# Performance work log

Hardware: AMD Instinct MI355X
Metric: run time of the kernel (lower is better)

The kernel has to match this reference:

```python
import jax, jax.numpy as jnp
from jax import lax
import numpy as np

BATCH, SEQ_LEN, ENC_IN, C_OUT = 16, 512, 32, 32
N_ORDER = 256           # window_size
MULTISCALE = (1, 2, 4)
MODES = min(32, SEQ_LEN // 2)  # = 32


def make_hippo(N, dt):
    """HiPPO-LegT transition, bilinear (Tustin) discretization, Legendre eval matrix."""
    Q = np.arange(N, dtype=np.float64)
    R = (2 * Q + 1)[:, None]
    j, i = np.meshgrid(Q, Q)
    A = np.where(i < j, -1.0, (-1.0) ** (i - j + 1)) * R
    B = (-1.0) ** Q[:, None] * R                      # [N,1]
    I = np.eye(N)
    M = I - (dt / 2.0) * A
    Ad = np.linalg.solve(M, I + (dt / 2.0) * A)
    Bd = np.linalg.solve(M, dt * B).squeeze(-1)       # [N]
    vals = np.arange(0.0, 1.0, dt)
    x = 1.0 - 2.0 * vals
    P = np.zeros((N, len(vals)))
    P[0] = 1.0
    if N > 1:
        P[1] = x
    for n in range(1, N - 1):
        P[n + 1] = ((2 * n + 1) * x * P[n] - n * P[n - 1]) / (n + 1)
    E = P.T                                           # [len(vals), N]
    return Ad.astype(np.float32), Bd.astype(np.float32), E.astype(np.float32)


def setup_inputs():
    key = jax.random.key(0)
    ks = jax.random.split(key, 12)
    inp = {}
    inp['x_enc'] = jax.random.normal(ks[0], (BATCH, SEQ_LEN, ENC_IN), jnp.float32)
    inp['x_mark_enc'] = jax.random.normal(ks[1], (BATCH, SEQ_LEN, 4), jnp.float32)
    inp['x_dec'] = jax.random.normal(ks[2], (BATCH, SEQ_LEN, ENC_IN), jnp.float32)
    inp['x_mark_dec'] = jax.random.normal(ks[3], (BATCH, SEQ_LEN, 4), jnp.float32)
    inp['affine_weight'] = jnp.ones((1, 1, ENC_IN), jnp.float32)
    inp['affine_bias'] = jnp.zeros((1, 1, ENC_IN), jnp.float32)
    scale = 1.0 / (N_ORDER * N_ORDER)
    for s in range(3):
        inp[f'wr{s}'] = scale * jax.random.uniform(ks[4 + 2 * s], (N_ORDER, N_ORDER, MODES), jnp.float32)
        inp[f'wi{s}'] = scale * jax.random.uniform(ks[5 + 2 * s], (N_ORDER, N_ORDER, MODES), jnp.float32)
    inp['mlp_w'] = 0.1 * jax.random.normal(ks[10], (1, 3), jnp.float32)
    inp['mlp_b'] = jnp.zeros((1,), jnp.float32)
    inp['proj_w'] = 0.02 * jax.random.normal(ks[11], (ENC_IN, C_OUT), jnp.float32)
    inp['proj_b'] = jnp.zeros((C_OUT,), jnp.float32)
    for s, m in enumerate(MULTISCALE):
        A, Bv, E = make_hippo(N_ORDER, 1.0 / SEQ_LEN / m)
        inp[f'A{s}'] = jnp.asarray(A)
        inp[f'Bv{s}'] = jnp.asarray(Bv)
        inp[f'E{s}'] = jnp.asarray(E)
    return inp


def _hippo_scan(x, A, Bv):
    # x: [B, L, C] -> cs: [L, B, C, N]; c_t = A c_{t-1} + B f_t (applied on last dim)
    B_, L, C = x.shape
    c0 = jnp.zeros((B_, C, A.shape[0]), x.dtype)
    At = A.T
    def step(c, f):                      # f: [B, C]
        c = c @ At + f[..., None] * Bv
        return c, c
    _, cs = lax.scan(step, c0, jnp.transpose(x, (1, 0, 2)))
    return cs


def _spectral_conv(xc, wr, wi):
    # xc: [B, C, N, L]; keep first MODES rfft bins, complex channel mix over N, irfft
    L = xc.shape[-1]
    xf = jnp.fft.rfft(xc)                                # [B,C,N,L//2+1] complex64
    W = (wr + 1j * wi).astype(jnp.complex64)             # [N,N,MODES]
    out = jnp.einsum('bjix,iox->bjox', xf[..., :MODES], W)
    out_ft = jnp.pad(out, ((0, 0), (0, 0), (0, 0), (0, L // 2 + 1 - MODES)))
    return jnp.fft.irfft(out_ft, n=L)                    # [B,C,N,L]


def _forward(x_enc, affine_weight, affine_bias, specs, mlp_w, mlp_b, proj_w, proj_b, hippos):
    means = lax.stop_gradient(jnp.mean(x_enc, axis=1, keepdims=True))
    xc = x_enc - means
    stdev = lax.stop_gradient(jnp.sqrt(jnp.var(xc, axis=1, keepdims=True) + 1e-5))
    x = xc / stdev
    x = x * affine_weight + affine_bias                  # [B, L, C]
    pred_len = SEQ_LEN
    decs = []
    for (wr, wi), (A, Bv, E) in zip(specs, hippos):
        # multiscale slice x[:, -m*pred_len:] clips to full seq_len since pred_len==seq_len
        cs = _hippo_scan(x, A, Bv)                       # [L,B,C,N]
        x_in_c = jnp.transpose(cs, (1, 2, 3, 0))         # [B,C,N,L]
        out1 = _spectral_conv(x_in_c, wr, wi)            # [B,C,N,L]
        x_dec_c = out1[..., pred_len - 1]                # [B,C,N]
        dec = x_dec_c @ E[-pred_len:, :].T               # [B,C,pred_len]
        decs.append(dec)
    stacked = jnp.stack(decs, axis=-1)                   # [B,C,P,3]
    y = stacked @ mlp_w[0] + mlp_b[0]                    # Linear(3,1) + squeeze -> [B,C,P]
    y = jnp.transpose(y, (0, 2, 1))                      # [B,P,C]
    y = (y - affine_bias) / (affine_weight + 1e-10)
    y = y * stdev + means
    return y @ proj_w + proj_b                           # OutputBlock: per-step channel projection


def reference(x_enc, x_mark_enc, x_dec, x_mark_dec, affine_weight, affine_bias,
              wr0, wi0, wr1, wi1, wr2, wi2, mlp_w, mlp_b, proj_w, proj_b,
              A0, Bv0, E0, A1, Bv1, E1, A2, Bv2, E2):
    specs = [(wr0, wi0), (wr1, wi1), (wr2, wi2)]
    hippos = [(A0, Bv0, E0), (A1, Bv1, E1), (A2, Bv2, E2)]
    return _forward(x_enc, affine_weight, affine_bias, specs, mlp_w, mlp_b, proj_w, proj_b, hippos)
```

## Files before the change

### kernel.cpp

```cpp
#include <hip/hip_runtime.h>
#include <math.h>

#define SEQ 512
#define NORD 256
#define MODES 32
#define KBIG (NORD*MODES*2)
#define PI_F 3.14159265358979323846f

typedef _Float16 half8 __attribute__((ext_vector_type(8)));
typedef float floatx4 __attribute__((ext_vector_type(4)));
typedef unsigned int uint;



struct GJob {
  const float* A; const float* B; float* C; const float* scale_ptr;
  int M, N, lda, k0, k1, atomic;
};
struct GJobs {
  GJob j[6];
  const float* wwr[3]; const float* wwi[3];
  _Float16* Wt; int nGemm; int wb_i0; int wb_slab0;
};

__global__ __launch_bounds__(256) void gemm32_k(GJobs P) {
  int z = blockIdx.z;
  if (z >= P.nGemm) {
    if (blockIdx.y != 0) return;
    int ig = P.wb_i0 + (z - P.nGemm);
    int s = ig >> 8, i = ig & 255;
    const float* wr = P.wwr[s];
    const float* wi = P.wwi[s];
    uint* Wd = (uint*)(P.Wt + (size_t)(s - P.wb_slab0) * 4194304);
    int j = blockIdx.x * 256 + threadIdx.x;
    int ot = j >> 7, loc = j & 127;
    int ks = loc >> 6, kg8 = (loc >> 4) & 3, on = loc & 15;
    int o = ot * 16 + on, k0 = ks * 16 + kg8 * 4;
    float4 wr4 = *(const float4*)&wr[(size_t)i * 8192 + o * 32 + k0];
    float4 wi4 = *(const float4*)&wi[(size_t)i * 8192 + o * 32 + k0];
    float wa[4] = {wr4.x, wr4.y, wr4.z, wr4.w};
    float wb[4] = {wi4.x, wi4.y, wi4.z, wi4.w};
    uint out[4];
    #pragma unroll
    for (int q = 0; q < 4; q++) {
      int k = k0 + q;
      float sn, cn; __sincosf((2.f * PI_F / 512.f) * (float)k, &sn, &cn);
      float g = ((k == 0) ? (1.f / 512.f) : (2.f / 512.f)) * 4096.f;
      float v0 = g * (cn * wa[q] + sn * wb[q]);
      float v1 = g * (sn * wa[q] - cn * wb[q]);
      _Float16 h0 = (_Float16)v0, h1 = (_Float16)v1;
      unsigned short u0, u1;
      __builtin_memcpy(&u0, &h0, 2); __builtin_memcpy(&u1, &h1, 2);
      out[q] = (uint)u0 | ((uint)u1 << 16);
    }
    *(uint4*)&Wd[((size_t)(i * 16 + ot)) * 512 + loc * 4] = *(uint4*)out;
    return;
  }
  GJob jb = P.j[z];
  int col0 = blockIdx.x * 32;
  int row0 = blockIdx.y * 32;
  if (row0 >= jb.M || col0 >= jb.N) return;
  __shared__ float As[64][34];
  __shared__ float Bs[64][36];
  int tid = threadIdx.x;
  int tx = tid & 15, ty = tid >> 4;
  const float* A = jb.A; const float* B = jb.B;
  int M = jb.M, N = jb.N, lda = jb.lda;
  int kcA = (tid & 15) * 4, rA = tid >> 4;
  int ccB = (tid & 7) * 4, kkB = tid >> 3;
  int gr0 = row0 + rA, gr1 = row0 + rA + 16;
  const float4 z4 = make_float4(0.f, 0.f, 0.f, 0.f);
  float4 a0, a1, b0, b1;
  {
    int kb = jb.k0;
    a0 = (gr0 < M) ? *(const float4*)&A[(size_t)gr0 * lda + kb + kcA] : z4;
    a1 = (gr1 < M) ? *(const float4*)&A[(size_t)gr1 * lda + kb + kcA] : z4;
    b0 = *(const float4*)&B[(size_t)(kb + kkB) * N + col0 + ccB];
    b1 = *(const float4*)&B[(size_t)(kb + kkB + 32) * N + col0 + ccB];
  }
  float acc00 = 0.f, acc01 = 0.f, acc10 = 0.f, acc11 = 0.f;
  for (int kb = jb.k0; kb < jb.k1; kb += 64) {
    As[kcA+0][rA] = a0.x; As[kcA+1][rA] = a0.y; As[kcA+2][rA] = a0.z; As[kcA+3][rA] = a0.w;
    As[kcA+0][rA+16] = a1.x; As[kcA+1][rA+16] = a1.y; As[kcA+2][rA+16] = a1.z; As[kcA+3][rA+16] = a1.w;
    *(float4*)&Bs[kkB][ccB] = b0;
    *(float4*)&Bs[kkB+32][ccB] = b1;
    __syncthreads();
    if (kb + 64 < jb.k1) {
      int kn = kb + 64;
      a0 = (gr0 < M) ? *(const float4*)&A[(size_t)gr0 * lda + kn + kcA] : z4;
      a1 = (gr1 < M) ? *(const float4*)&A[(size_t)gr1 * lda + kn + kcA] : z4;
      b0 = *(const float4*)&B[(size_t)(kn + kkB) * N + col0 + ccB];
      b1 = *(const float4*)&B[(size_t)(kn + kkB + 32) * N + col0 + ccB];
    }
    #pragma unroll
    for (int k = 0; k < 64; k++) {
      float2 av = *(float2*)&As[k][ty * 2];
      float2 bv = *(float2*)&Bs[k][tx * 2];
      acc00 += av.x * bv.x; acc01 += av.x * bv.y;
      acc10 += av.y * bv.x; acc11 += av.y * bv.y;
    }
    __syncthreads();
  }
  float sc = jb.scale_ptr ? *jb.scale_ptr : 1.f;
  int gr = row0 + ty * 2, gc = col0 + tx * 2;
  float v00 = acc00 * sc, v01 = acc01 * sc, v10 = acc10 * sc, v11 = acc11 * sc;
  if (jb.atomic) {
    if (gr < M)     { atomicAdd(&jb.C[(size_t)gr * N + gc], v00);     atomicAdd(&jb.C[(size_t)gr * N + gc + 1], v01); }
    if (gr + 1 < M) { atomicAdd(&jb.C[(size_t)(gr+1) * N + gc], v10); atomicAdd(&jb.C[(size_t)(gr+1) * N + gc + 1], v11); }
  } else {
    if (gr < M)     { jb.C[(size_t)gr * N + gc] = v00;     jb.C[(size_t)gr * N + gc + 1] = v01; }
    if (gr + 1 < M) { jb.C[(size_t)(gr+1) * N + gc] = v10; jb.C[(size_t)(gr+1) * N + gc + 1] = v11; }
  }
}


__global__ __launch_bounds__(256) void setup_k(const float* A0, const float* A1, const float* A2,
                                               const float* B0, const float* B1, const float* B2,
                                               const float* E0, const float* E1, const float* E2,
                                               const float* x, const float* aw, const float* ab,
                                               float* R, float* Kry, float* Et, float* Z,
                                               float* F, float* stats) {
  long bid = blockIdx.x;
  int tid = threadIdx.x;
  if (bid < 768) {
    long idx = bid * 256 + tid;
    int scl = (int)(idx >> 16);
    int r = (int)(idx & 65535);
    int m = r >> 8, i2 = r & 255;
    const float* A = scl == 0 ? A0 : (scl == 1 ? A1 : A2);
    R[(size_t)scl * 2 * 65536 + (size_t)m * 256 + i2] = A[(size_t)i2 * 256 + m];
  } else if (bid < 2304) {
    long idx = (bid - 768) * 256 + tid;
    int scl = (int)(idx / 131072);
    int r = (int)(idx % 131072);
    int p = r >> 8, o = r & 255;
    const float* E; int rows;
    if (scl == 0) { E = E0; rows = 512; }
    else if (scl == 1) { E = E1; rows = 1024; }
    else { E = E2; rows = 2048; }
    int base = rows - 512;
    Et[(size_t)scl * 131072 + (size_t)o * 512 + p] = E[(size_t)(base + p) * 256 + o];
  } else if (bid < 2307) {
    int scl = (int)(bid - 2304);
    const float* B = scl == 0 ? B0 : (scl == 1 ? B1 : B2);
    Kry[(size_t)scl * 131072 + tid] = B[tid];
  } else if (bid < 4867) {
    long idx = (bid - 2307) * 256 + tid;
    if (idx < 655360) Z[idx] = 0.f;
  } else {
    int row = (int)(bid - 4867);
    int b = row >> 5, c = row & 31;
    const float* xp = x + (size_t)b * SEQ * 32 + c;
    float v0 = xp[(size_t)tid * 32];
    float v1 = xp[(size_t)(tid + 256) * 32];
    float s = v0 + v1, s2 = v0 * v0 + v1 * v1;
    for (int off = 32; off; off >>= 1) {
      s  += __shfl_down(s,  off, 64);
      s2 += __shfl_down(s2, off, 64);
    }
    __shared__ float ws1[4], ws2[4];
    __shared__ float mean_s, istd_s;
    int wid = tid >> 6, lane = tid & 63;
    if (lane == 0) { ws1[wid] = s; ws2[wid] = s2; }
    __syncthreads();
    if (tid == 0) {
      float t1 = ws1[0] + ws1[1] + ws1[2] + ws1[3];
      float t2 = ws2[0] + ws2[1] + ws2[2] + ws2[3];
      float mean = t1 / 512.f;
      float var = t2 / 512.f - mean * mean;
      float sd = sqrtf(var + 1e-5f);
      mean_s = mean; istd_s = 1.f / sd;
      stats[row] = mean; stats[512 + row] = sd;
    }
    __syncthreads();
    float w = aw[c], bb = ab[c];
    float m = mean_s, is = istd_s;
    F[(size_t)row * SEQ + tid]       = (v0 - m) * is * w + bb;
    F[(size_t)row * SEQ + tid + 256] = (v1 - m) * is * w + bb;
  }
}


__global__ __launch_bounds__(256) void qbuildA_k(const float* __restrict__ Kry,
                                                 float2* __restrict__ Pp, int s0) {
  int bg = blockIdx.x;
  int s = s0 + (bg >> 8);
  int r = bg & 255;
  int k = r & 31, c = r >> 5;
  const float* Kry_s = Kry + (size_t)s * 131072;
  float2* P = Pp + (size_t)s * 65536;
  int i = threadIdx.x;
  float ar = 0.f, ai = 0.f;
  const float step = 2.f * PI_F / 512.f;
  int m0 = c * 64;
  for (int mm = 0; mm < 64; mm++) {
    int m = m0 + mm;
    float kap = Kry_s[(size_t)m * 256 + i];
    float sn, cn; __sincosf(step * (float)((k * m) & 511), &sn, &cn);
    ar += kap * cn; ai -= kap * sn;
  }
  P[(size_t)(c * 32 + k) * 256 + i] = make_float2(ar, ai);
}


__global__ __launch_bounds__(256) void qbuildB_k(const float* __restrict__ Kry,
                                                 const float2* __restrict__ Pp,
                                                 _Float16* __restrict__ Qf, int s0) {
  int bg = blockIdx.x;
  int slab = bg >> 8;
  int s = s0 + slab;
  int r = bg & 255;
  int ig = r & 31, c = r >> 5;
  const float* Kry_s = Kry + (size_t)s * 131072;
  const float2* P = Pp + (size_t)s * 65536;
  uint* Qd = (uint*)(Qf + (size_t)slab * 8388608);
  int tid = threadIdx.x;
  int k = tid & 31, il = tid >> 5;
  int i = ig * 8 + il;
  __shared__ __align__(16) uint buf[16 * 260];
  float ar = 0.f, ai = 0.f;
  for (int cp = 0; cp < c; cp++) {
    float2 p = P[(size_t)(cp * 32 + k) * 256 + i];
    ar += p.x; ai += p.y;
  }
  const float step = 2.f * PI_F / 512.f;
  int m0 = c * 64;
  int u = tid & 31, myil = tid >> 5;
  for (int mb = 0; mb < 64; mb += 16) {
    #pragma unroll
    for (int mm = 0; mm < 16; mm++) {
      int m = m0 + mb + mm;
      float kap = Kry_s[(size_t)m * 256 + i];
      float sn, cn; __sincosf(step * (float)((k * m) & 511), &sn, &cn);
      ar += kap * cn; ai -= kap * sn;
      int st = 511 - m;
      float sn2, cn2; __sincosf(step * (float)((k * st) & 511), &sn2, &cn2);
      float qr = ar * cn2 + ai * sn2;
      float qi = ai * cn2 - ar * sn2;
      qr = fminf(fmaxf(qr, -60000.f), 60000.f);
      qi = fminf(fmaxf(qi, -60000.f), 60000.f);
      _Float16 h0 = (_Float16)qr, h1 = (_Float16)qi;
      unsigned short u0, u1;
      __builtin_memcpy(&u0, &h0, 2); __builtin_memcpy(&u1, &h1, 2);
      buf[(st & 15) * 260 + il * 32 + k] = (uint)u0 | ((uint)u1 << 16);
    }
    __syncthreads();
    int stt = (511 - (m0 + mb)) >> 4;
    int kc = ig * 8 + myil;
    uint* tile = Qd + ((size_t)(kc * 32 + stt)) * 512;
    #pragma unroll
    for (int r4 = 0; r4 < 4; r4++) {
      int f = u * 4 + r4;
      int m = f & 15, kg8 = (f >> 4) & 3, ks = f >> 6;
      uint4 v = *(uint4*)&buf[m * 260 + myil * 32 + ks * 16 + kg8 * 4];
      *(uint4*)&tile[f * 4] = v;
    }
    __syncthreads();
  }
}


__global__ __launch_bounds__(256) void umfma_k(const _Float16* __restrict__ Qf,
                                               const _Float16* __restrict__ Wt,
                                               float* __restrict__ U, int s0) {
  __shared__ __align__(16) uint Al_u[4096];
  __shared__ __align__(16) uint Bl_u[4096];
  int slab = blockIdx.z >> 4;
  int kslab = blockIdx.z & 15;
  int s = s0 + slab;
  const uint* Qt = (const uint*)(Qf + (size_t)slab * 8388608);
  const uint* Wu = (const uint*)(Wt + (size_t)slab * 4194304);
  float* Us = U + (size_t)s * 131072;
  int stt0 = blockIdx.x * 8;
  int ot0 = blockIdx.y * 8;
  int m0 = blockIdx.x * 128, n0 = blockIdx.y * 128;
  int tid = threadIdx.x;
  int w = tid >> 6, lane = tid & 63;
  int quad = lane >> 4, lm = lane & 15;
  floatx4 acc[4][4];
  #pragma unroll
  for (int a = 0; a < 4; a++)
    #pragma unroll
    for (int b = 0; b < 4; b++) acc[a][b] = (floatx4)(0.f);
  int wmt = (w & 1) * 4, wnt = (w >> 1) * 4;
  uint4 qa[4], qb[4];
  {
    int kc = kslab * 16;
    const uint* qsrc = Qt + ((size_t)(kc * 32 + stt0)) * 512;
    const uint* wsrc = Wu + ((size_t)(kc * 16 + ot0)) * 512;
    #pragma unroll
    for (int r = 0; r < 4; r++) {
      qa[r] = *(const uint4*)&qsrc[(r * 256 + tid) * 4];
      qb[r] = *(const uint4*)&wsrc[(r * 256 + tid) * 4];
    }
  }
  for (int it = 0; it < 16; it++) {
    __syncthreads();
    #pragma unroll
    for (int r = 0; r < 4; r++) {
      *(uint4*)&Al_u[(r * 256 + tid) * 4] = qa[r];
      *(uint4*)&Bl_u[(r * 256 + tid) * 4] = qb[r];
    }
    __syncthreads();
    if (it < 15) {
      int kc = kslab * 16 + it + 1;
      const uint* qsrc = Qt + ((size_t)(kc * 32 + stt0)) * 512;
      const uint* wsrc = Wu + ((size_t)(kc * 16 + ot0)) * 512;
      #pragma unroll
      for (int r = 0; r < 4; r++) {
        qa[r] = *(const uint4*)&qsrc[(r * 256 + tid) * 4];
        qb[r] = *(const uint4*)&wsrc[(r * 256 + tid) * 4];
      }
    }
    #pragma unroll
    for (int ks = 0; ks < 2; ks++) {
      half8 af[4], bf[4];
      #pragma unroll
      for (int t = 0; t < 4; t++) {
        af[t] = *(half8*)((_Float16*)Al_u + ((wmt + t) * 1024 + ks * 512 + lane * 8));
        bf[t] = *(half8*)((_Float16*)Bl_u + ((wnt + t) * 1024 + ks * 512 + lane * 8));
      }
      #pragma unroll
      for (int mi = 0; mi < 4; mi++)
        #pragma unroll
        for (int ni = 0; ni < 4; ni++)
          acc[mi][ni] = __builtin_amdgcn_mfma_f32_16x16x32_f16(af[mi], bf[ni], acc[mi][ni], 0, 0, 0);
    }
  }
  #pragma unroll
  for (int mi = 0; mi < 4; mi++) {
    int gr0 = m0 + wmt * 16 + mi * 16 + quad * 4;
    #pragma unroll
    for (int ni = 0; ni < 4; ni++) {
      int gc = n0 + wnt * 16 + ni * 16 + lm;
      #pragma unroll
      for (int r = 0; r < 4; r++)
        atomicAdd(&Us[(size_t)(gr0 + r) * 256 + gc], acc[mi][ni][r] * (1.f / 4096.f));
    }
  }
}


__global__ __launch_bounds__(256) void y0final_k(const float* __restrict__ F,
                                                 const float* __restrict__ Ttot,
                                                 const float* __restrict__ stats,
                                                 const float* __restrict__ aw,
                                                 const float* __restrict__ ab,
                                                 const float* __restrict__ mlp_b,
                                                 const float* __restrict__ pw,
                                                 const float* __restrict__ pb,
                                                 float* __restrict__ out) {
  __shared__ float As[64][34];
  __shared__ float Bs[64][36];
  __shared__ float ys[32][33];
  __shared__ float pws[1024];
  int bxp = blockIdx.x;
  int b = blockIdx.y;
  int row0 = b * 32, col0 = bxp * 32;
  int tid = threadIdx.x;
  for (int t = tid; t < 1024; t += 256) pws[t] = pw[t];
  int tx = tid & 15, ty = tid >> 4;
  int kcA = (tid & 15) * 4, rA = tid >> 4;
  int ccB = (tid & 7) * 4, kkB = tid >> 3;
  int gr0 = row0 + rA, gr1 = row0 + rA + 16;
  float4 a0, a1, b0, b1;
  a0 = *(const float4*)&F[(size_t)gr0 * 512 + kcA];
  a1 = *(const float4*)&F[(size_t)gr1 * 512 + kcA];
  b0 = *(const float4*)&Ttot[(size_t)kkB * 512 + col0 + ccB];
  b1 = *(const float4*)&Ttot[(size_t)(kkB + 32) * 512 + col0 + ccB];
  float acc00 = 0.f, acc01 = 0.f, acc10 = 0.f, acc11 = 0.f;
  for (int kb = 0; kb < 512; kb += 64) {
    As[kcA+0][rA] = a0.x; As[kcA+1][rA] = a0.y; As[kcA+2][rA] = a0.z; As[kcA+3][rA] = a0.w;
    As[kcA+0][rA+16] = a1.x; As[kcA+1][rA+16] = a1.y; As[kcA+2][rA+16] = a1.z; As[kcA+3][rA+16] = a1.w;
    *(float4*)&Bs[kkB][ccB] = b0;
    *(float4*)&Bs[kkB+32][ccB] = b1;
    __syncthreads();
    if (kb + 64 < 512) {
      int kn = kb + 64;
      a0 = *(const float4*)&F[(size_t)gr0 * 512 + kn + kcA];
      a1 = *(const float4*)&F[(size_t)gr1 * 512 + kn + kcA];
      b0 = *(const float4*)&Ttot[(size_t)(kn + kkB) * 512 + col0 + ccB];
      b1 = *(const float4*)&Ttot[(size_t)(kn + kkB + 32) * 512 + col0 + ccB];
    }
    #pragma unroll
    for (int k = 0; k < 64; k++) {
      float2 av = *(float2*)&As[k][ty * 2];
      float2 bv = *(float2*)&Bs[k][tx * 2];
      acc00 += av.x * bv.x; acc01 += av.x * bv.y;
      acc10 += av.y * bv.x; acc11 += av.y * bv.y;
    }
    __syncthreads();
  }
  float mb0 = mlp_b[0];
  {
    int c0 = ty * 2, c1 = ty * 2 + 1;
    int r0g = row0 + c0, r1g = row0 + c1;
    float mean0 = stats[r0g], sd0 = stats[512 + r0g];
    float mean1 = stats[r1g], sd1 = stats[512 + r1g];
    float q0 = sd0 / (aw[c0] + 1e-10f), q1 = sd1 / (aw[c1] + 1e-10f);
    float o0 = mean0 - (ab[c0] - mb0) * q0, o1 = mean1 - (ab[c1] - mb0) * q1;
    ys[c0][tx * 2]     = acc00 * q0 + o0;
    ys[c0][tx * 2 + 1] = acc01 * q0 + o0;
    ys[c1][tx * 2]     = acc10 * q1 + o1;
    ys[c1][tx * 2 + 1] = acc11 * q1 + o1;
  }
  __syncthreads();
  int p = tid >> 3, co0 = (tid & 7) * 4;
  float4 facc = *(const float4*)&pb[co0];
  #pragma unroll
  for (int cc = 0; cc < 32; cc++) {
    float f = ys[cc][p];
    float4 pw4 = *(float4*)&pws[cc * 32 + co0];
    facc.x += f * pw4.x; facc.y += f * pw4.y; facc.z += f * pw4.z; facc.w += f * pw4.w;
  }
  *(float4*)&out[(size_t)b * 16384 + (size_t)(col0 + p) * 32 + co0] = facc;
}


extern "C" void kernel_launch(void* const* d_in, const int* in_sizes, int n_in,
                              void* d_out, int out_size, void* d_ws, size_t ws_size,
                              hipStream_t stream) {
  const float* x_enc = (const float*)d_in[0];
  const float* aw = (const float*)d_in[4];
  const float* ab = (const float*)d_in[5];
  const float* wr[3] = {(const float*)d_in[6], (const float*)d_in[8], (const float*)d_in[10]};
  const float* wi[3] = {(const float*)d_in[7], (const float*)d_in[9], (const float*)d_in[11]};
  const float* mlp_w = (const float*)d_in[12];
  const float* mlp_b = (const float*)d_in[13];
  const float* proj_w = (const float*)d_in[14];
  const float* proj_b = (const float*)d_in[15];
  const float* Am[3]  = {(const float*)d_in[16], (const float*)d_in[19], (const float*)d_in[22]};
  const float* Bv[3]  = {(const float*)d_in[17], (const float*)d_in[20], (const float*)d_in[23]};
  const float* Em[3]  = {(const float*)d_in[18], (const float*)d_in[21], (const float*)d_in[24]};

  float* w = (float*)d_ws;
  float* F     = w; w += 512 * 512;
  float* stats = w; w += 1024;
  float* Kry   = w; w += 3 * 512 * 256;
  float* R     = w; w += 3 * 2 * 65536;
  float* U     = w; w += 3 * 512 * 256;
  float* Ttot  = w; w += 512 * 512;
  float* Et    = w; w += 3 * 256 * 512;
  float* Pp    = w; w += 3 * 65536 * 2;
  _Float16* Qf = (_Float16*)w;

  size_t base_bytes = (size_t)((char*)Qf - (char*)d_ws);
  size_t slab_bytes = (size_t)(8388608 + 4194304) * 2;
  int nS = (ws_size >= base_bytes + 3 * slab_bytes) ? 3 : 1;
  _Float16* Wb = Qf + (size_t)nS * 8388608;

  setup_k<<<5379, 256, 0, stream>>>(Am[0], Am[1], Am[2], Bv[0], Bv[1], Bv[2],
                                    Em[0], Em[1], Em[2], x_enc, aw, ab,
                                    R, Kry, Et, U, F, stats);

  int wb_done = 0;
  for (int j = 0; j < 9; j++) {
    GJobs P{};
    int M = 1 << j;
    int cur = j & 1;
    int nz = 0;
    for (int s = 0; s < 3; s++) {
      float* Ks = Kry + (size_t)s * 131072;
      float* Rj = R + (size_t)s * 131072 + (size_t)cur * 65536;
      float* Rn = R + (size_t)s * 131072 + (size_t)(1 - cur) * 65536;
      P.j[nz++] = {Ks, Rj, Ks + (size_t)M * 256, nullptr, M, 256, 256, 0, 256, 0};
      if (j < 8) P.j[nz++] = {Rj, Rj, Rn, nullptr, 256, 256, 256, 0, 256, 0};
    }
    P.nGemm = nz;
    int wb_cnt = 0;
    if (nS == 3) {
      wb_cnt = (j < 8) ? 86 : (768 - 86 * 8);
      P.wwr[0] = wr[0]; P.wwr[1] = wr[1]; P.wwr[2] = wr[2];
      P.wwi[0] = wi[0]; P.wwi[1] = wi[1]; P.wwi[2] = wi[2];
      P.Wt = Wb; P.wb_i0 = wb_done; P.wb_slab0 = 0;
      wb_done += wb_cnt;
    }
    gemm32_k<<<dim3(8, 8, nz + wb_cnt), 256, 0, stream>>>(P);
  }

  if (nS == 3) {
    qbuildA_k<<<768, 256, 0, stream>>>(Kry, (float2*)Pp, 0);
    qbuildB_k<<<768, 256, 0, stream>>>(Kry, (const float2*)Pp, Qf, 0);
    umfma_k<<<dim3(4, 2, 48), 256, 0, stream>>>(Qf, Wb, U, 0);
  } else {
    for (int s = 0; s < 3; s++) {
      GJobs P{};
      P.nGemm = 0;
      P.wwr[0] = wr[0]; P.wwr[1] = wr[1]; P.wwr[2] = wr[2];
      P.wwi[0] = wi[0]; P.wwi[1] = wi[1]; P.wwi[2] = wi[2];
      P.Wt = Wb; P.wb_i0 = s * 256; P.wb_slab0 = s;
      gemm32_k<<<dim3(8, 1, 256), 256, 0, stream>>>(P);
      qbuildA_k<<<256, 256, 0, stream>>>(Kry, (float2*)Pp, s);
      qbuildB_k<<<256, 256, 0, stream>>>(Kry, (const float2*)Pp, Qf, s);
      umfma_k<<<dim3(4, 2, 16), 256, 0, stream>>>(Qf, Wb, U, s);
    }
  }

  {
    GJobs P{};
    for (int s = 0; s < 3; s++)
      P.j[s] = {U + (size_t)s * 131072, Et + (size_t)s * 131072, Ttot,
                mlp_w + s, 512, 512, 256, 0, 256, 1};
    P.nGemm = 3;
    gemm32_k<<<dim3(16, 16, 3), 256, 0, stream>>>(P);
  }

  y0final_k<<<dim3(16, 16), 256, 0, stream>>>(F, Ttot, stats, aw, ab, mlp_b,
                                              proj_w, proj_b, (float*)d_out);
}
```

Measured before the change: 399.2 us.

## Fuse launch chains into persistent kernels with device-wide atomic barriers

The per-level GEMM launches of the power-doubling chain are replaced by a single persistent chain_k kernel that loops over levels and synchronises with an atomic grid barrier. qbuildA/qbuildB become one kernel (qab_k), and the Ttot GEMM and final projection become one kernel (tty0_k), each joined by a grid barrier. The W-transform work moves into setup_k. umfma_k gets an XCD-aware block remapping, and the U zeroing is shortened because atomic accumulation is no longer used. The aim is to remove launch overhead and tail idle time between dependent launches. The grid barriers depend on every block being co-resident, so they can deadlock if occupancy falls short, and the small-M chain levels leave most blocks idle.

Result: slower. 781.4 us (+95.7%).

```diff
diff --git a/kernel.cpp b/kernel.cpp
--- a/kernel.cpp
+++ b/kernel.cpp
@@ -12,80 +12,43 @@
 typedef unsigned int uint;
 
 
-
-struct GJob {
-  const float* A; const float* B; float* C; const float* scale_ptr;
-  int M, N, lda, k0, k1, atomic;
-};
-struct GJobs {
-  GJob j[6];
-  const float* wwr[3]; const float* wwi[3];
-  _Float16* Wt; int nGemm; int wb_i0; int wb_slab0;
-};
-
-__global__ __launch_bounds__(256) void gemm32_k(GJobs P) {
-  int z = blockIdx.z;
-  if (z >= P.nGemm) {
-    if (blockIdx.y != 0) return;
-    int ig = P.wb_i0 + (z - P.nGemm);
-    int s = ig >> 8, i = ig & 255;
-    const float* wr = P.wwr[s];
-    const float* wi = P.wwi[s];
-    uint* Wd = (uint*)(P.Wt + (size_t)(s - P.wb_slab0) * 4194304);
-    int j = blockIdx.x * 256 + threadIdx.x;
-    int ot = j >> 7, loc = j & 127;
-    int ks = loc >> 6, kg8 = (loc >> 4) & 3, on = loc & 15;
-    int o = ot * 16 + on, k0 = ks * 16 + kg8 * 4;
-    float4 wr4 = *(const float4*)&wr[(size_t)i * 8192 + o * 32 + k0];
-    float4 wi4 = *(const float4*)&wi[(size_t)i * 8192 + o * 32 + k0];
-    float wa[4] = {wr4.x, wr4.y, wr4.z, wr4.w};
-    float wb[4] = {wi4.x, wi4.y, wi4.z, wi4.w};
-    uint out[4];
-    #pragma unroll
-    for (int q = 0; q < 4; q++) {
-      int k = k0 + q;
-      float sn, cn; __sincosf((2.f * PI_F / 512.f) * (float)k, &sn, &cn);
-      float g = ((k == 0) ? (1.f / 512.f) : (2.f / 512.f)) * 4096.f;
-      float v0 = g * (cn * wa[q] + sn * wb[q]);
-      float v1 = g * (sn * wa[q] - cn * wb[q]);
-      _Float16 h0 = (_Float16)v0, h1 = (_Float16)v1;
-      unsigned short u0, u1;
-      __builtin_memcpy(&u0, &h0, 2); __builtin_memcpy(&u1, &h1, 2);
-      out[q] = (uint)u0 | ((uint)u1 << 16);
-    }
-    *(uint4*)&Wd[((size_t)(i * 16 + ot)) * 512 + loc * 4] = *(uint4*)out;
-    return;
-  }
-  GJob jb = P.j[z];
-  int col0 = blockIdx.x * 32;
-  int row0 = blockIdx.y * 32;
-  if (row0 >= jb.M || col0 >= jb.N) return;
-  __shared__ float As[64][34];
-  __shared__ float Bs[64][36];
+__device__ __forceinline__ void gbar(int* cnt, int target) {
+  __syncthreads();
+  if (threadIdx.x == 0) {
+    __hip_atomic_fetch_add(cnt, 1, __ATOMIC_ACQ_REL, __HIP_MEMORY_SCOPE_AGENT);
+    while (__hip_atomic_load(cnt, __ATOMIC_ACQUIRE, __HIP_MEMORY_SCOPE_AGENT) < target)
+      __builtin_amdgcn_s_sleep(8);
+  }
+  __syncthreads();
+}
+
+
+__device__ __forceinline__ void gemm_tile(const float* __restrict__ A,
+                                          const float* __restrict__ B,
+                                          int M, int N, int lda, int K,
+                                          int row0, int col0, float ascale,
+                                          float (*As)[34], float (*Bs)[36],
+                                          float* acc) {
   int tid = threadIdx.x;
   int tx = tid & 15, ty = tid >> 4;
-  const float* A = jb.A; const float* B = jb.B;
-  int M = jb.M, N = jb.N, lda = jb.lda;
   int kcA = (tid & 15) * 4, rA = tid >> 4;
   int ccB = (tid & 7) * 4, kkB = tid >> 3;
   int gr0 = row0 + rA, gr1 = row0 + rA + 16;
   const float4 z4 = make_float4(0.f, 0.f, 0.f, 0.f);
   float4 a0, a1, b0, b1;
-  {
-    int kb = jb.k0;
-    a0 = (gr0 < M) ? *(const float4*)&A[(size_t)gr0 * lda + kb + kcA] : z4;
-    a1 = (gr1 < M) ? *(const float4*)&A[(size_t)gr1 * lda + kb + kcA] : z4;
-    b0 = *(const float4*)&B[(size_t)(kb + kkB) * N + col0 + ccB];
-    b1 = *(const float4*)&B[(size_t)(kb + kkB + 32) * N + col0 + ccB];
-  }
-  float acc00 = 0.f, acc01 = 0.f, acc10 = 0.f, acc11 = 0.f;
-  for (int kb = jb.k0; kb < jb.k1; kb += 64) {
-    As[kcA+0][rA] = a0.x; As[kcA+1][rA] = a0.y; As[kcA+2][rA] = a0.z; As[kcA+3][rA] = a0.w;
-    As[kcA+0][rA+16] = a1.x; As[kcA+1][rA+16] = a1.y; As[kcA+2][rA+16] = a1.z; As[kcA+3][rA+16] = a1.w;
+  a0 = (gr0 < M) ? *(const float4*)&A[(size_t)gr0 * lda + kcA] : z4;
+  a1 = (gr1 < M) ? *(const float4*)&A[(size_t)gr1 * lda + kcA] : z4;
+  b0 = *(const float4*)&B[(size_t)kkB * N + col0 + ccB];
+  b1 = *(const float4*)&B[(size_t)(kkB + 32) * N + col0 + ccB];
+  for (int kb = 0; kb < K; kb += 64) {
+    As[kcA+0][rA] = a0.x * ascale; As[kcA+1][rA] = a0.y * ascale;
+    As[kcA+2][rA] = a0.z * ascale; As[kcA+3][rA] = a0.w * ascale;
+    As[kcA+0][rA+16] = a1.x * ascale; As[kcA+1][rA+16] = a1.y * ascale;
+    As[kcA+2][rA+16] = a1.z * ascale; As[kcA+3][rA+16] = a1.w * ascale;
     *(float4*)&Bs[kkB][ccB] = b0;
     *(float4*)&Bs[kkB+32][ccB] = b1;
     __syncthreads();
-    if (kb + 64 < jb.k1) {
+    if (kb + 64 < K) {
       int kn = kb + 64;
       a0 = (gr0 < M) ? *(const float4*)&A[(size_t)gr0 * lda + kn + kcA] : z4;
       a1 = (gr1 < M) ? *(const float4*)&A[(size_t)gr1 * lda + kn + kcA] : z4;
@@ -96,20 +59,10 @@
     for (int k = 0; k < 64; k++) {
       float2 av = *(float2*)&As[k][ty * 2];
       float2 bv = *(float2*)&Bs[k][tx * 2];
-      acc00 += av.x * bv.x; acc01 += av.x * bv.y;
-      acc10 += av.y * bv.x; acc11 += av.y * bv.y;
-    }
-    __syncthreads();
-  }
-  float sc = jb.scale_ptr ? *jb.scale_ptr : 1.f;
-  int gr = row0 + ty * 2, gc = col0 + tx * 2;
-  float v00 = acc00 * sc, v01 = acc01 * sc, v10 = acc10 * sc, v11 = acc11 * sc;
-  if (jb.atomic) {
-    if (gr < M)     { atomicAdd(&jb.C[(size_t)gr * N + gc], v00);     atomicAdd(&jb.C[(size_t)gr * N + gc + 1], v01); }
-    if (gr + 1 < M) { atomicAdd(&jb.C[(size_t)(gr+1) * N + gc], v10); atomicAdd(&jb.C[(size_t)(gr+1) * N + gc + 1], v11); }
-  } else {
-    if (gr < M)     { jb.C[(size_t)gr * N + gc] = v00;     jb.C[(size_t)gr * N + gc + 1] = v01; }
-    if (gr + 1 < M) { jb.C[(size_t)(gr+1) * N + gc] = v10; jb.C[(size_t)(gr+1) * N + gc + 1] = v11; }
+      acc[0] += av.x * bv.x; acc[1] += av.x * bv.y;
+      acc[2] += av.y * bv.x; acc[3] += av.y * bv.y;
+    }
+    __syncthreads();
   }
 }
 
@@ -118,8 +71,11 @@
                                                const float* B0, const float* B1, const float* B2,
                                                const float* E0, const float* E1, const float* E2,
                                                const float* x, const float* aw, const float* ab,
+                                               const float* wr0, const float* wi0,
+                                               const float* wr1, const float* wi1,
+                                               const float* wr2, const float* wi2,
                                                float* R, float* Kry, float* Et, float* Z,
-                                               float* F, float* stats) {
+                                               float* F, float* stats, _Float16* Wb, int* bar) {
   long bid = blockIdx.x;
   int tid = threadIdx.x;
   if (bid < 768) {
@@ -144,11 +100,11 @@
     int scl = (int)(bid - 2304);
     const float* B = scl == 0 ? B0 : (scl == 1 ? B1 : B2);
     Kry[(size_t)scl * 131072 + tid] = B[tid];
-  } else if (bid < 4867) {
+  } else if (bid < 3843) {
     long idx = (bid - 2307) * 256 + tid;
-    if (idx < 655360) Z[idx] = 0.f;
-  } else {
-    int row = (int)(bid - 4867);
+    Z[idx] = 0.f;
+  } else if (bid < 4355) {
+    int row = (int)(bid - 3843);
     int b = row >> 5, c = row & 31;
     const float* xp = x + (size_t)b * SEQ * 32 + c;
     float v0 = xp[(size_t)tid * 32];
@@ -177,103 +133,175 @@
     float m = mean_s, is = istd_s;
     F[(size_t)row * SEQ + tid]       = (v0 - m) * is * w + bb;
     F[(size_t)row * SEQ + tid + 256] = (v1 - m) * is * w + bb;
-  }
-}
-
-
-__global__ __launch_bounds__(256) void qbuildA_k(const float* __restrict__ Kry,
-                                                 float2* __restrict__ Pp, int s0) {
+  } else if (bid == 4355) {
+    if (tid < 64) bar[tid] = 0;
+  } else {
+    long u = bid - 4356;
+    int ig = (int)(u >> 3), sub = (int)(u & 7);
+    int s = ig >> 8, i = ig & 255;
+    const float* wr = s == 0 ? wr0 : (s == 1 ? wr1 : wr2);
+    const float* wi = s == 0 ? wi0 : (s == 1 ? wi1 : wi2);
+    uint* Wd = (uint*)(Wb + (size_t)s * 4194304);
+    int jj = sub * 256 + tid;
+    int ot = jj >> 7, loc = jj & 127;
+    int ks = loc >> 6, kg8 = (loc >> 4) & 3, on = loc & 15;
+    int o = ot * 16 + on, k0 = ks * 16 + kg8 * 4;
+    float4 wr4 = *(const float4*)&wr[(size_t)i * 8192 + o * 32 + k0];
+    float4 wi4 = *(const float4*)&wi[(size_t)i * 8192 + o * 32 + k0];
+    float wa[4] = {wr4.x, wr4.y, wr4.z, wr4.w};
+    float wb[4] = {wi4.x, wi4.y, wi4.z, wi4.w};
+    uint outv[4];
+    #pragma unroll
+    for (int q = 0; q < 4; q++) {
+      int k = k0 + q;
+      float sn, cn; __sincosf((2.f * PI_F / 512.f) * (float)k, &sn, &cn);
+      float g = ((k == 0) ? (1.f / 512.f) : (2.f / 512.f)) * 4096.f;
+      float v0 = g * (cn * wa[q] + sn * wb[q]);
+      float v1 = g * (sn * wa[q] - cn * wb[q]);
+      _Float16 h0 = (_Float16)v0, h1 = (_Float16)v1;
+      unsigned short u0, u1;
+      __builtin_memcpy(&u0, &h0, 2); __builtin_memcpy(&u1, &h1, 2);
+      outv[q] = (uint)u0 | ((uint)u1 << 16);
+    }
+    *(uint4*)&Wd[((size_t)(i * 16 + ot)) * 512 + loc * 4] = *(uint4*)outv;
+  }
+}
+
+
+__global__ __launch_bounds__(256, 2) void chain_k(float* Kry, float* R, int* bar) {
+  __shared__ float As[64][34];
+  __shared__ float Bs[64][36];
+  int tid = threadIdx.x;
+  for (int j = 0; j < 9; j++) {
+    int M = 1 << j;
+    int cur = j & 1;
+    int rta = (M + 31) >> 5;
+    int ta = rta * 8;
+    int nApp = 3 * ta;
+    int ntiles = nApp + ((j < 8) ? 192 : 0);
+    for (int t = blockIdx.x; t < ntiles; t += gridDim.x) {
+      const float *A, *B; float* C; int Mj, row0, col0;
+      if (t < nApp) {
+        int s = t / ta, lt = t - s * ta;
+        int rt = lt >> 3, ct = lt & 7;
+        float* Ks = Kry + (size_t)s * 131072;
+        A = Ks;
+        B = R + (size_t)s * 131072 + (size_t)cur * 65536;
+        C = Ks + (size_t)M * 256;
+        Mj = M; row0 = rt * 32; col0 = ct * 32;
+      } else {
+        int t2 = t - nApp;
+        int s = t2 >> 6, lt = t2 & 63;
+        int rt = lt >> 3, ct = lt & 7;
+        float* Rj = R + (size_t)s * 131072 + (size_t)cur * 65536;
+        A = Rj; B = Rj;
+        C = R + (size_t)s * 131072 + (size_t)(1 - cur) * 65536;
+        Mj = 256; row0 = rt * 32; col0 = ct * 32;
+      }
+      float acc[4] = {0.f, 0.f, 0.f, 0.f};
+      gemm_tile(A, B, Mj, 256, 256, 256, row0, col0, 1.f, As, Bs, acc);
+      int tx = tid & 15, ty = tid >> 4;
+      int gr = row0 + ty * 2, gc = col0 + tx * 2;
+      if (gr < Mj)     { C[(size_t)gr * 256 + gc] = acc[0];     C[(size_t)gr * 256 + gc + 1] = acc[1]; }
+      if (gr + 1 < Mj) { C[(size_t)(gr+1) * 256 + gc] = acc[2]; C[(size_t)(gr+1) * 256 + gc + 1] = acc[3]; }
+    }
+    if (j < 8) gbar(bar, (int)gridDim.x * (j + 1));
+  }
+}
+
+
+__global__ __launch_bounds__(256, 3) void qab_k(const float* __restrict__ Kry,
+                                                float2* __restrict__ Pp,
+                                                _Float16* __restrict__ Qf, int* bar) {
+  __shared__ __align__(16) uint buf[16 * 260];
   int bg = blockIdx.x;
-  int s = s0 + (bg >> 8);
-  int r = bg & 255;
-  int k = r & 31, c = r >> 5;
-  const float* Kry_s = Kry + (size_t)s * 131072;
-  float2* P = Pp + (size_t)s * 65536;
-  int i = threadIdx.x;
-  float ar = 0.f, ai = 0.f;
+  int tid = threadIdx.x;
   const float step = 2.f * PI_F / 512.f;
-  int m0 = c * 64;
-  for (int mm = 0; mm < 64; mm++) {
-    int m = m0 + mm;
-    float kap = Kry_s[(size_t)m * 256 + i];
-    float sn, cn; __sincosf(step * (float)((k * m) & 511), &sn, &cn);
-    ar += kap * cn; ai -= kap * sn;
-  }
-  P[(size_t)(c * 32 + k) * 256 + i] = make_float2(ar, ai);
-}
-
-
-__global__ __launch_bounds__(256) void qbuildB_k(const float* __restrict__ Kry,
-                                                 const float2* __restrict__ Pp,
-                                                 _Float16* __restrict__ Qf, int s0) {
-  int bg = blockIdx.x;
-  int slab = bg >> 8;
-  int s = s0 + slab;
-  int r = bg & 255;
-  int ig = r & 31, c = r >> 5;
-  const float* Kry_s = Kry + (size_t)s * 131072;
-  const float2* P = Pp + (size_t)s * 65536;
-  uint* Qd = (uint*)(Qf + (size_t)slab * 8388608);
-  int tid = threadIdx.x;
-  int k = tid & 31, il = tid >> 5;
-  int i = ig * 8 + il;
-  __shared__ __align__(16) uint buf[16 * 260];
-  float ar = 0.f, ai = 0.f;
-  for (int cp = 0; cp < c; cp++) {
-    float2 p = P[(size_t)(cp * 32 + k) * 256 + i];
-    ar += p.x; ai += p.y;
-  }
-  const float step = 2.f * PI_F / 512.f;
-  int m0 = c * 64;
-  int u = tid & 31, myil = tid >> 5;
-  for (int mb = 0; mb < 64; mb += 16) {
-    #pragma unroll
-    for (int mm = 0; mm < 16; mm++) {
-      int m = m0 + mb + mm;
+  {
+    int s = bg >> 8;
+    int r = bg & 255;
+    int k = r & 31, c = r >> 5;
+    const float* Kry_s = Kry + (size_t)s * 131072;
+    float2* P = Pp + (size_t)s * 65536;
+    int i = tid;
+    float ar = 0.f, ai = 0.f;
+    int m0 = c * 64;
+    for (int mm = 0; mm < 64; mm++) {
+      int m = m0 + mm;
       float kap = Kry_s[(size_t)m * 256 + i];
       float sn, cn; __sincosf(step * (float)((k * m) & 511), &sn, &cn);
       ar += kap * cn; ai -= kap * sn;
-      int st = 511 - m;
-      float sn2, cn2; __sincosf(step * (float)((k * st) & 511), &sn2, &cn2);
-      float qr = ar * cn2 + ai * sn2;
-      float qi = ai * cn2 - ar * sn2;
-      qr = fminf(fmaxf(qr, -60000.f), 60000.f);
-      qi = fminf(fmaxf(qi, -60000.f), 60000.f);
-      _Float16 h0 = (_Float16)qr, h1 = (_Float16)qi;
-      unsigned short u0, u1;
-      __builtin_memcpy(&u0, &h0, 2); __builtin_memcpy(&u1, &h1, 2);
-      buf[(st & 15) * 260 + il * 32 + k] = (uint)u0 | ((uint)u1 << 16);
-    }
-    __syncthreads();
-    int stt = (511 - (m0 + mb)) >> 4;
-    int kc = ig * 8 + myil;
-    uint* tile = Qd + ((size_t)(kc * 32 + stt)) * 512;
-    #pragma unroll
-    for (int r4 = 0; r4 < 4; r4++) {
-      int f = u * 4 + r4;
-      int m = f & 15, kg8 = (f >> 4) & 3, ks = f >> 6;
-      uint4 v = *(uint4*)&buf[m * 260 + myil * 32 + ks * 16 + kg8 * 4];
-      *(uint4*)&tile[f * 4] = v;
-    }
-    __syncthreads();
-  }
-}
-
-
-__global__ __launch_bounds__(256) void umfma_k(const _Float16* __restrict__ Qf,
-                                               const _Float16* __restrict__ Wt,
-                                               float* __restrict__ U, int s0) {
+    }
+    P[(size_t)(c * 32 + k) * 256 + i] = make_float2(ar, ai);
+  }
+  gbar(bar, (int)gridDim.x);
+  {
+    int slab = bg >> 8;
+    int r = bg & 255;
+    int ig = r & 31, c = r >> 5;
+    const float* Kry_s = Kry + (size_t)slab * 131072;
+    const float2* P = Pp + (size_t)slab * 65536;
+    uint* Qd = (uint*)(Qf + (size_t)slab * 8388608);
+    int k = tid & 31, il = tid >> 5;
+    int i = ig * 8 + il;
+    float ar = 0.f, ai = 0.f;
+    for (int cp = 0; cp < c; cp++) {
+      float2 p = P[(size_t)(cp * 32 + k) * 256 + i];
+      ar += p.x; ai += p.y;
+    }
+    int m0 = c * 64;
+    int u = tid & 31, myil = tid >> 5;
+    for (int mb = 0; mb < 64; mb += 16) {
+      #pragma unroll
+      for (int mm = 0; mm < 16; mm++) {
+        int m = m0 + mb + mm;
+        float kap = Kry_s[(size_t)m * 256 + i];
+        float sn, cn; __sincosf(step * (float)((k * m) & 511), &sn, &cn);
+        ar += kap * cn; ai -= kap * sn;
+        int st = 511 - m;
+        float sn2, cn2; __sincosf(step * (float)((k * st) & 511), &sn2, &cn2);
+        float qr = ar * cn2 + ai * sn2;
+        float qi = ai * cn2 - ar * sn2;
+        qr = fminf(fmaxf(qr, -60000.f), 60000.f);
+        qi = fminf(fmaxf(qi, -60000.f), 60000.f);
+        _Float16 h0 = (_Float16)qr, h1 = (_Float16)qi;
+        unsigned short u0, u1;
+        __builtin_memcpy(&u0, &h0, 2); __builtin_memcpy(&u1, &h1, 2);
+        buf[(st & 15) * 260 + il * 32 + k] = (uint)u0 | ((uint)u1 << 16);
+      }
+      __syncthreads();
+      int stt = (511 - (m0 + mb)) >> 4;
+      int kc = ig * 8 + myil;
+      uint* tile = Qd + ((size_t)(kc * 32 + stt)) * 512;
+      #pragma unroll
+      for (int r4 = 0; r4 < 4; r4++) {
+        int f = u * 4 + r4;
+        int m = f & 15, kg8 = (f >> 4) & 3, ks = f >> 6;
+        uint4 v = *(uint4*)&buf[m * 260 + myil * 32 + ks * 16 + kg8 * 4];
+        *(uint4*)&tile[f * 4] = v;
+      }
+      __syncthreads();
+    }
+  }
+}
+
+
+__global__ __launch_bounds__(256, 3) void umfma_k(const _Float16* __restrict__ Qf,
+                                                  const _Float16* __restrict__ Wt,
+                                                  float* __restrict__ U) {
   __shared__ __align__(16) uint Al_u[4096];
   __shared__ __align__(16) uint Bl_u[4096];
-  int slab = blockIdx.z >> 4;
-  int kslab = blockIdx.z & 15;
-  int s = s0 + slab;
+  int Fb = blockIdx.x;
+  int xcd = Fb & 7, jj = Fb >> 3;
+  int g = (jj >> 3) * 8 + xcd;
+  int mem = jj & 7;
+  int slab = g >> 5, ks = g & 31;
+  int mx = mem & 3, ny = mem >> 2;
   const uint* Qt = (const uint*)(Qf + (size_t)slab * 8388608);
   const uint* Wu = (const uint*)(Wt + (size_t)slab * 4194304);
-  float* Us = U + (size_t)s * 131072;
-  int stt0 = blockIdx.x * 8;
-  int ot0 = blockIdx.y * 8;
-  int m0 = blockIdx.x * 128, n0 = blockIdx.y * 128;
+  float* Us = U + (size_t)slab * 131072;
+  int stt0 = mx * 8, ot0 = ny * 8;
+  int m0 = mx * 128, n0 = ny * 128;
   int tid = threadIdx.x;
   int w = tid >> 6, lane = tid & 63;
   int quad = lane >> 4, lm = lane & 15;
@@ -285,7 +313,7 @@
   int wmt = (w & 1) * 4, wnt = (w >> 1) * 4;
   uint4 qa[4], qb[4];
   {
-    int kc = kslab * 16;
+    int kc = ks * 8;
     const uint* qsrc = Qt + ((size_t)(kc * 32 + stt0)) * 512;
     const uint* wsrc = Wu + ((size_t)(kc * 16 + ot0)) * 512;
     #pragma unroll
@@ -294,7 +322,7 @@
       qb[r] = *(const uint4*)&wsrc[(r * 256 + tid) * 4];
     }
   }
-  for (int it = 0; it < 16; it++) {
+  for (int it = 0; it < 8; it++) {
     __syncthreads();
     #pragma unroll
     for (int r = 0; r < 4; r++) {
@@ -302,8 +330,8 @@
       *(uint4*)&Bl_u[(r * 256 + tid) * 4] = qb[r];
     }
     __syncthreads();
-    if (it < 15) {
-      int kc = kslab * 16 + it + 1;
+    if (it < 7) {
+      int kc = ks * 8 + it + 1;
       const uint* qsrc = Qt + ((size_t)(kc * 32 + stt0)) * 512;
       const uint* wsrc = Wu + ((size_t)(kc * 16 + ot0)) * 512;
       #pragma unroll
@@ -313,12 +341,12 @@
       }
     }
     #pragma unroll
-    for (int ks = 0; ks < 2; ks++) {
+    for (int kss = 0; kss < 2; kss++) {
       half8 af[4], bf[4];
       #pragma unroll
       for (int t = 0; t < 4; t++) {
-        af[t] = *(half8*)((_Float16*)Al_u + ((wmt + t) * 1024 + ks * 512 + lane * 8));
-        bf[t] = *(half8*)((_Float16*)Bl_u + ((wnt + t) * 1024 + ks * 512 + lane * 8));
+        af[t] = *(half8*)((_Float16*)Al_u + ((wmt + t) * 1024 + kss * 512 + lane * 8));
+        bf[t] = *(half8*)((_Float16*)Bl_u + ((wnt + t) * 1024 + kss * 512 + lane * 8));
       }
       #pragma unroll
       for (int mi = 0; mi < 4; mi++)
@@ -341,79 +369,65 @@
 }
 
 
-__global__ __launch_bounds__(256) void y0final_k(const float* __restrict__ F,
-                                                 const float* __restrict__ Ttot,
-                                                 const float* __restrict__ stats,
-                                                 const float* __restrict__ aw,
-                                                 const float* __restrict__ ab,
-                                                 const float* __restrict__ mlp_b,
-                                                 const float* __restrict__ pw,
-                                                 const float* __restrict__ pb,
-                                                 float* __restrict__ out) {
+__global__ __launch_bounds__(256) void tty0_k(const float* __restrict__ U,
+                                              const float* __restrict__ Et,
+                                              const float* __restrict__ mlp_w,
+                                              float* __restrict__ Ttot,
+                                              const float* __restrict__ F,
+                                              const float* __restrict__ stats,
+                                              const float* __restrict__ aw,
+                                              const float* __restrict__ ab,
+                                              const float* __restrict__ mlp_b,
+                                              const float* __restrict__ pw,
+                                              const float* __restrict__ pb,
+                                              float* __restrict__ out, int* bar) {
   __shared__ float As[64][34];
   __shared__ float Bs[64][36];
   __shared__ float ys[32][33];
   __shared__ float pws[1024];
-  int bxp = blockIdx.x;
-  int b = blockIdx.y;
-  int row0 = b * 32, col0 = bxp * 32;
-  int tid = threadIdx.x;
+  int tid = threadIdx.x;
+  int tx = tid & 15, ty = tid >> 4;
   for (int t = tid; t < 1024; t += 256) pws[t] = pw[t];
-  int tx = tid & 15, ty = tid >> 4;
-  int kcA = (tid & 15) * 4, rA = tid >> 4;
-  int ccB = (tid & 7) * 4, kkB = tid >> 3;
-  int gr0 = row0 + rA, gr1 = row0 + rA + 16;
-  float4 a0, a1, b0, b1;
-  a0 = *(const float4*)&F[(size_t)gr0 * 512 + kcA];
-  a1 = *(const float4*)&F[(size_t)gr1 * 512 + kcA];
-  b0 = *(const float4*)&Ttot[(size_t)kkB * 512 + col0 + ccB];
-  b1 = *(const float4*)&Ttot[(size_t)(kkB + 32) * 512 + col0 + ccB];
-  float acc00 = 0.f, acc01 = 0.f, acc10 = 0.f, acc11 = 0.f;
-  for (int kb = 0; kb < 512; kb += 64) {
-    As[kcA+0][rA] = a0.x; As[kcA+1][rA] = a0.y; As[kcA+2][rA] = a0.z; As[kcA+3][rA] = a0.w;
-    As[kcA+0][rA+16] = a1.x; As[kcA+1][rA+16] = a1.y; As[kcA+2][rA+16] = a1.z; As[kcA+3][rA+16] = a1.w;
-    *(float4*)&Bs[kkB][ccB] = b0;
-    *(float4*)&Bs[kkB+32][ccB] = b1;
-    __syncthreads();
-    if (kb + 64 < 512) {
-      int kn = kb + 64;
-      a0 = *(const float4*)&F[(size_t)gr0 * 512 + kn + kcA];
-      a1 = *(const float4*)&F[(size_t)gr1 * 512 + kn + kcA];
-      b0 = *(const float4*)&Ttot[(size_t)(kn + kkB) * 512 + col0 + ccB];
-      b1 = *(const float4*)&Ttot[(size_t)(kn + kkB + 32) * 512 + col0 + ccB];
-    }
-    #pragma unroll
-    for (int k = 0; k < 64; k++) {
-      float2 av = *(float2*)&As[k][ty * 2];
-      float2 bv = *(float2*)&Bs[k][tx * 2];
-      acc00 += av.x * bv.x; acc01 += av.x * bv.y;
-      acc10 += av.y * bv.x; acc11 += av.y * bv.y;
-    }
-    __syncthreads();
-  }
-  float mb0 = mlp_b[0];
   {
-    int c0 = ty * 2, c1 = ty * 2 + 1;
+    int lt = blockIdx.x;
+    int rt = lt >> 4, ct = lt & 15;
+    int row0 = rt * 32, col0 = ct * 32;
+    float acc[4] = {0.f, 0.f, 0.f, 0.f};
+    for (int s = 0; s < 3; s++)
+      gemm_tile(U + (size_t)s * 131072, Et + (size_t)s * 131072,
+                512, 512, 256, 256, row0, col0, mlp_w[s], As, Bs, acc);
+    int gr = row0 + ty * 2, gc = col0 + tx * 2;
+    Ttot[(size_t)gr * 512 + gc] = acc[0];       Ttot[(size_t)gr * 512 + gc + 1] = acc[1];
+    Ttot[(size_t)(gr+1) * 512 + gc] = acc[2];   Ttot[(size_t)(gr+1) * 512 + gc + 1] = acc[3];
+  }
+  gbar(bar, (int)gridDim.x);
+  {
+    int bxp = blockIdx.x & 15, bb = blockIdx.x >> 4;
+    int row0 = bb * 32, col0 = bxp * 32;
+    float acc[4] = {0.f, 0.f, 0.f, 0.f};
+    gemm_tile(F, Ttot, 512, 512, 512, 512, row0, col0, 1.f, As, Bs, acc);
+    float mb0 = mlp_b[0];
+    int c0 = ty * 2, c1 = c0 + 1;
     int r0g = row0 + c0, r1g = row0 + c1;
     float mean0 = stats[r0g], sd0 = stats[512 + r0g];
     float mean1 = stats[r1g], sd1 = stats[512 + r1g];
     float q0 = sd0 / (aw[c0] + 1e-10f), q1 = sd1 / (aw[c1] + 1e-10f);
     float o0 = mean0 - (ab[c0] - mb0) * q0, o1 = mean1 - (ab[c1] - mb0) * q1;
-    ys[c0][tx * 2]     = acc00 * q0 + o0;
-    ys[c0][tx * 2 + 1] = acc01 * q0 + o0;
-    ys[c1][tx * 2]     = acc10 * q1 + o1;
-    ys[c1][tx * 2 + 1] = acc11 * q1 + o1;
-  }
-  __syncthreads();
-  int p = tid >> 3, co0 = (tid & 7) * 4;
-  float4 facc = *(const float4*)&pb[co0];
-  #pragma unroll
-  for (int cc = 0; cc < 32; cc++) {
-    float f = ys[cc][p];
-    float4 pw4 = *(float4*)&pws[cc * 32 + co0];
-    facc.x += f * pw4.x; facc.y += f * pw4.y; facc.z += f * pw4.z; facc.w += f * pw4.w;
-  }
-  *(float4*)&out[(size_t)b * 16384 + (size_t)(col0 + p) * 32 + co0] = facc;
+    ys[c0][tx * 2]     = acc[0] * q0 + o0;
+    ys[c0][tx * 2 + 1] = acc[1] * q0 + o0;
+    ys[c1][tx * 2]     = acc[2] * q1 + o1;
+    ys[c1][tx * 2 + 1] = acc[3] * q1 + o1;
+    __syncthreads();
+    int p = tid >> 3, co0 = (tid & 7) * 4;
+    float4 facc = *(const float4*)&pb[co0];
+    #pragma unroll
+    for (int cc = 0; cc < 32; cc++) {
+      float f = ys[cc][p];
+      float4 pw4 = *(float4*)&pws[cc * 32 + co0];
+      facc.x += f * pw4.x; facc.y += f * pw4.y; facc.z += f * pw4.z; facc.w += f * pw4.w;
+    }
+    *(float4*)&out[(size_t)bb * 16384 + (size_t)(col0 + p) * 32 + co0] = facc;
+  }
 }
 
 
@@ -436,75 +450,23 @@
   float* w = (float*)d_ws;
   float* F     = w; w += 512 * 512;
   float* stats = w; w += 1024;
-  float* Kry   = w; w += 3 * 512 * 256;
-  float* R     = w; w += 3 * 2 * 65536;
-  float* U     = w; w += 3 * 512 * 256;
+  float* Kry   = w; w += 3 * 131072;
+  float* R     = w; w += 3 * 131072;
+  float* U     = w; w += 3 * 131072;
   float* Ttot  = w; w += 512 * 512;
-  float* Et    = w; w += 3 * 256 * 512;
-  float* Pp    = w; w += 3 * 65536 * 2;
+  float* Et    = w; w += 3 * 131072;
+  float* Pp    = w; w += 3 * 131072;
+  int*   bar   = (int*)w; w += 64;
   _Float16* Qf = (_Float16*)w;
-
-  size_t base_bytes = (size_t)((char*)Qf - (char*)d_ws);
-  size_t slab_bytes = (size_t)(8388608 + 4194304) * 2;
-  int nS = (ws_size >= base_bytes + 3 * slab_bytes) ? 3 : 1;
-  _Float16* Wb = Qf + (size_t)nS * 8388608;
-
-  setup_k<<<5379, 256, 0, stream>>>(Am[0], Am[1], Am[2], Bv[0], Bv[1], Bv[2],
-                                    Em[0], Em[1], Em[2], x_enc, aw, ab,
-                                    R, Kry, Et, U, F, stats);
-
-  int wb_done = 0;
-  for (int j = 0; j < 9; j++) {
-    GJobs P{};
-    int M = 1 << j;
-    int cur = j & 1;
-    int nz = 0;
-    for (int s = 0; s < 3; s++) {
-      float* Ks = Kry + (size_t)s * 131072;
-      float* Rj = R + (size_t)s * 131072 + (size_t)cur * 65536;
-      float* Rn = R + (size_t)s * 131072 + (size_t)(1 - cur) * 65536;
-      P.j[nz++] = {Ks, Rj, Ks + (size_t)M * 256, nullptr, M, 256, 256, 0, 256, 0};
-      if (j < 8) P.j[nz++] = {Rj, Rj, Rn, nullptr, 256, 256, 256, 0, 256, 0};
-    }
-    P.nGemm = nz;
-    int wb_cnt = 0;
-    if (nS == 3) {
-      wb_cnt = (j < 8) ? 86 : (768 - 86 * 8);
-      P.wwr[0] = wr[0]; P.wwr[1] = wr[1]; P.wwr[2] = wr[2];
-      P.wwi[0] = wi[0]; P.wwi[1] = wi[1]; P.wwi[2] = wi[2];
-      P.Wt = Wb; P.wb_i0 = wb_done; P.wb_slab0 = 0;
-      wb_done += wb_cnt;
-    }
-    gemm32_k<<<dim3(8, 8, nz + wb_cnt), 256, 0, stream>>>(P);
-  }
-
-  if (nS == 3) {
-    qbuildA_k<<<768, 256, 0, stream>>>(Kry, (float2*)Pp, 0);
-    qbuildB_k<<<768, 256, 0, stream>>>(Kry, (const float2*)Pp, Qf, 0);
-    umfma_k<<<dim3(4, 2, 48), 256, 0, stream>>>(Qf, Wb, U, 0);
-  } else {
-    for (int s = 0; s < 3; s++) {
-      GJobs P{};
-      P.nGemm = 0;
-      P.wwr[0] = wr[0]; P.wwr[1] = wr[1]; P.wwr[2] = wr[2];
-      P.wwi[0] = wi[0]; P.wwi[1] = wi[1]; P.wwi[2] = wi[2];
-      P.Wt = Wb; P.wb_i0 = s * 256; P.wb_slab0 = s;
-      gemm32_k<<<dim3(8, 1, 256), 256, 0, stream>>>(P);
-      qbuildA_k<<<256, 256, 0, stream>>>(Kry, (float2*)Pp, s);
-      qbuildB_k<<<256, 256, 0, stream>>>(Kry, (const float2*)Pp, Qf, s);
-      umfma_k<<<dim3(4, 2, 16), 256, 0, stream>>>(Qf, Wb, U, s);
-    }
-  }
-
-  {
-    GJobs P{};
-    for (int s = 0; s < 3; s++)
-      P.j[s] = {U + (size_t)s * 131072, Et + (size_t)s * 131072, Ttot,
-                mlp_w + s, 512, 512, 256, 0, 256, 1};
-    P.nGemm = 3;
-    gemm32_k<<<dim3(16, 16, 3), 256, 0, stream>>>(P);
-  }
-
-  y0final_k<<<dim3(16, 16), 256, 0, stream>>>(F, Ttot, stats, aw, ab, mlp_b,
-                                              proj_w, proj_b, (float*)d_out);
-}
+  _Float16* Wb = Qf + (size_t)3 * 8388608;
+
+  setup_k<<<10500, 256, 0, stream>>>(Am[0], Am[1], Am[2], Bv[0], Bv[1], Bv[2],
+                                     Em[0], Em[1], Em[2], x_enc, aw, ab,
+                                     wr[0], wi[0], wr[1], wi[1], wr[2], wi[2],
+                                     R, Kry, Et, U, F, stats, Wb, bar);
+  chain_k<<<384, 256, 0, stream>>>(Kry, R, bar + 0);
+  qab_k<<<768, 256, 0, stream>>>(Kry, (float2*)Pp, Qf, bar + 16);
+  umfma_k<<<768, 256, 0, stream>>>(Qf, Wb, U);
+  tty0_k<<<256, 256, 0, stream>>>(U, Et, mlp_w, Ttot, F, stats, aw, ab, mlp_b,
+                                  proj_w, proj_b, (float*)d_out, bar + 32);
+}
```
